# Performance work log

Measured on AMD Instinct MI355X. Metric: run time of the kernel, lower is better.

## Reference

```python
import jax, jax.numpy as jnp
import numpy as np
from math import factorial

DEGREES = 6
REP = 10
PROJ = 64
R = 0.8
B = DEGREES + 1          # bandwidth; spherical signal grid is (2B, 2B)
M = (DEGREES + 1) ** 2   # 49 spherical-harmonic coefficients

# ---------- Wigner small-d coefficient tables (numpy, per degree) ----------

def _wigner_terms(l):
    idx_mp, idx_m, coef, pc, ps = [], [], [], [], []
    for mp in range(-l, l + 1):
        for m in range(-l, l + 1):
            pref = np.sqrt(float(factorial(l + mp) * factorial(l - mp) * factorial(l + m) * factorial(l - m)))
            for k in range(max(0, m - mp), min(l + m, l - mp) + 1):
                c = ((-1.0) ** (mp - m + k)) * pref / (
                    factorial(l + m - k) * factorial(k) * factorial(l - mp - k) * factorial(mp - m + k))
                idx_mp.append(mp + l); idx_m.append(m + l); coef.append(c)
                pc.append(2 * l + m - mp - 2 * k); ps.append(mp - m + 2 * k)
    return (np.asarray(idx_mp), np.asarray(idx_m), np.asarray(coef, np.float32),
            np.asarray(pc, np.float32), np.asarray(ps, np.float32))

_TERMS = [_wigner_terms(l) for l in range(DEGREES + 1)]


def _wigner_d(l, beta):
    """Real Wigner small-d matrix d^l_{m',m}(beta): (n, 2l+1, 2l+1)."""
    imp, im, coef, pc, ps = _TERMS[l]
    c = jnp.cos(beta / 2)[:, None]
    s = jnp.sin(beta / 2)[:, None]
    t = coef[None] * (c ** pc[None]) * (s ** ps[None])   # (n, T)
    d = jnp.zeros((beta.shape[0], 2 * l + 1, 2 * l + 1), beta.dtype)
    return d.at[:, imp, im].add(t)


def rotate_spectrum(angles, spectrum):
    """Block-diagonal complex Wigner-D multiply.
    angles: (n,3) ZYZ Euler; spectrum: (M, rep, 2) -> (Sre, Sim) each (n, M, rep)."""
    alpha, beta, gamma = angles[:, 0], angles[:, 1], angles[:, 2]
    out_re, out_im = [], []
    for l in range(DEGREES + 1):
        d = _wigner_d(l, beta)                                    # (n, 2l+1, 2l+1)
        ms = jnp.arange(-l, l + 1, dtype=angles.dtype)
        ang = ms[None, :, None] * alpha[:, None, None] + ms[None, None, :] * gamma[:, None, None]
        Dre = d * jnp.cos(ang)
        Dim = -d * jnp.sin(ang)                                   # D = e^{-i m' a} d e^{-i m g}
        blk = spectrum[l * l:(l + 1) * (l + 1)]                   # (2l+1, rep, 2)
        Sre, Sim = blk[..., 0], blk[..., 1]
        out_re.append(jnp.einsum('nij,jr->nir', Dre, Sre) - jnp.einsum('nij,jr->nir', Dim, Sim))
        out_im.append(jnp.einsum('nij,jr->nir', Dre, Sim) + jnp.einsum('nij,jr->nir', Dim, Sre))
    return jnp.concatenate(out_re, 1), jnp.concatenate(out_im, 1)


# ---------- Spherical harmonic synthesis table (numpy constant) ----------

def _sph_harm_table():
    J = 2 * B
    betas = np.pi * (2 * np.arange(J) + 1) / (4 * B)
    alphas = 2 * np.pi * np.arange(J) / J
    x, sx = np.cos(betas), np.sin(betas)
    L = DEGREES
    P = np.zeros((L + 1, L + 1, J))   # associated Legendre P[l, m] (Condon-Shortley)
    P[0, 0] = 1.0
    for m in range(1, L + 1):
        P[m, m] = -(2 * m - 1) * sx * P[m - 1, m - 1]
    for m in range(L + 1):
        if m + 1 <= L:
            P[m + 1, m] = (2 * m + 1) * x * P[m, m]
        for l in range(m + 2, L + 1):
            P[l, m] = ((2 * l - 1) * x * P[l - 1, m] - (l + m - 1) * P[l - 2, m]) / (l - m)
    Yre = np.zeros((M, J, J)); Yim = np.zeros((M, J, J))
    for l in range(L + 1):
        for m in range(0, l + 1):
            N = np.sqrt((2 * l + 1) / (4 * np.pi) * factorial(l - m) / factorial(l + m))
            pr = N * P[l, m]
            yre = pr[:, None] * np.cos(m * alphas)[None, :]
            yim = pr[:, None] * np.sin(m * alphas)[None, :]
            Yre[l * l + l + m], Yim[l * l + l + m] = yre, yim
            if m > 0:
                sgn = (-1.0) ** m
                Yre[l * l + l - m], Yim[l * l + l - m] = sgn * yre, -sgn * yim
    return jnp.asarray(Yre, jnp.float32), jnp.asarray(Yim, jnp.float32)

_YRE, _YIM = _sph_harm_table()


def s2_ifft_real(Sre, Sim):
    """f(beta,alpha) = Re[sum_lm c_lm Y_lm]: (n, rep, 2B, 2B)."""
    return jnp.einsum('nmr,mjk->nrjk', Sre, _YRE) - jnp.einsum('nmr,mjk->nrjk', Sim, _YIM)


# ---------- Orthographic sampling grid (numpy constant) ----------

def _ortho_grid(h, w, r):
    ys, xs = np.meshgrid(np.linspace(-r, r, h), np.linspace(-r, r, w), indexing='ij')
    rho = np.sqrt(xs ** 2 + ys ** 2)
    theta = np.arcsin(np.clip(rho, 0.0, 1.0))     # colatitude of front hemisphere
    phi = np.arctan2(ys, xs)                      # longitude in [-pi, pi)
    gx = phi / np.pi                              # alpha axis  -> grid x
    gy = 2 * theta / np.pi - 1                    # beta axis   -> grid y
    return jnp.asarray(np.stack([gx, gy], -1), jnp.float32)

_GRID = _ortho_grid(PROJ, PROJ, R)


def grid_sample_bilinear(img, grid):
    """F.grid_sample(mode=bilinear, padding=zeros, align_corners=False).
    img: (n,C,H,W); grid: (Ho,Wo,2) shared across batch."""
    n, C, H, W = img.shape
    gx = (grid[..., 0] + 1) * W / 2 - 0.5
    gy = (grid[..., 1] + 1) * H / 2 - 0.5
    x0 = jnp.floor(gx); y0 = jnp.floor(gy)
    wx1 = gx - x0; wx0 = 1 - wx1
    wy1 = gy - y0; wy0 = 1 - wy1

    def gather(xi, yi, w):
        valid = (xi >= 0) & (xi < W) & (yi >= 0) & (yi < H)
        xc = jnp.clip(xi, 0, W - 1).astype(jnp.int32)
        yc = jnp.clip(yi, 0, H - 1).astype(jnp.int32)
        vals = img[:, :, yc, xc]                 # (n, C, Ho, Wo)
        return vals * (w * valid)[None, None]
    return (gather(x0, y0, wx0 * wy0) + gather(x0 + 1, y0, wx1 * wy0)
            + gather(x0, y0 + 1, wx0 * wy1) + gather(x0 + 1, y0 + 1, wx1 * wy1))


def deconv_apply(x, wt, bt):
    """ConvTranspose2d(REP,1,kernel=4,stride=2,padding=1); wt torch layout (Cin,Cout,4,4)."""
    k = jnp.transpose(wt[:, :, ::-1, ::-1], (1, 0, 2, 3))   # (Cout,Cin,kh,kw), flipped
    y = jax.lax.conv_general_dilated(x, k, window_strides=(1, 1),
                                     padding=((2, 2), (2, 2)), lhs_dilation=(2, 2),
                                     dimension_numbers=('NCHW', 'OIHW', 'NCHW'))
    return y + bt[None, :, None, None]


def setup_inputs() -> dict:
    key = jax.random.key(0)
    k1, k2, k3 = jax.random.split(key, 3)
    return {
        'angles': jax.random.uniform(k1, (2048, 3), dtype=jnp.float32),
        'spectrum': jax.random.normal(k2, (M, REP, 2), dtype=jnp.float32),
        'wt': jax.random.normal(k3, (REP, 1, 4, 4), dtype=jnp.float32) * 0.1,
        'bt': jnp.zeros((1,), jnp.float32),
    }


def reference(angles, spectrum, wt, bt):
    Sre, Sim = rotate_spectrum(angles, spectrum)        # (n, M, rep) complex parts
    signal = s2_ifft_real(Sre, Sim)                     # (n, rep, 14, 14)
    projection = grid_sample_bilinear(signal, _GRID)    # (n, rep, 64, 64)
    return deconv_apply(projection, wt, bt)             # (n, 1, 128, 128)
```

## Files before the change

kernel.cpp:

```cpp
#include <hip/hip_runtime.h>
#include <math.h>

#define DEG   6
#define MM    49
#define REPC  10
#define JD    14
#define JROWS 8
#define PROJD 64

#define PI_F 3.14159265358979323846f
#define PI_D 3.14159265358979323846

#define WS_GW    0
#define WS_GIDX  17424
#define WS_PT    21780
#define WS_CS    22172
#define WS_FLAG  22368
#define INIT_MAGIC 0x5F3A9C71u

__device__ __constant__ int DOFF[8] = {0,1,10,35,84,165,286,455};
__device__ __constant__ float FACTF[13] = {
    1.f,1.f,2.f,6.f,24.f,120.f,720.f,5040.f,40320.f,362880.f,
    3628800.f,39916800.f,479001600.f};
__device__ __constant__ double FACTD[13] = {
    1.,1.,2.,6.,24.,120.,720.,5040.,40320.,362880.,3628800.,39916800.,479001600.};

__device__ inline float ipowf(float b, int e) {
    float r = 1.f, p = b;
    while (e) { if (e & 1) r *= p; p *= p; e >>= 1; }
    return r;
}

__global__ void init_tables(float* __restrict__ ws) {
    if (*(const volatile unsigned int*)(ws + WS_FLAG) == INIT_MAGIC) return;
    const int tid = blockIdx.x * 256 + threadIdx.x;

    if (tid < 4356) {
        const int ty = tid / 66, tx = tid - ty * 66;
        const int iy = ty - 1, ix = tx - 1;
        float4 wv = make_float4(0.f, 0.f, 0.f, 0.f);
        unsigned int bidx = 0u;
        if ((unsigned)iy < 64u && (unsigned)ix < 64u) {
            float ys = -0.8f + 1.6f * (float)iy / 63.f;
            float xs = -0.8f + 1.6f * (float)ix / 63.f;
            float rho = sqrtf(xs * xs + ys * ys);
            float theta = asinf(fminf(rho, 1.0f));
            float phi = atan2f(ys, xs);
            float gxp = (phi / PI_F + 1.f) * 7.f - 0.5f;
            float gyp = (2.f * theta / PI_F) * 7.f - 0.5f;
            float x0f = floorf(gxp), y0f = floorf(gyp);
            int x0 = (int)x0f, y0 = (int)y0f;
            float fx = gxp - x0f, fy = gyp - y0f;
            float wx0 = 1.f - fx, wx1 = fx, wy0 = 1.f - fy, wy1 = fy;
            int xb = x0, yb = y0;
            if (x0 < 0)            { xb = 0; wx0 = wx1; wx1 = 0.f; }
            else if (x0 >= JD - 1) { wx1 = 0.f; }
            if (y0 < 0)            { yb = 0; wy0 = wy1; wy1 = 0.f; }
            wv = make_float4(wy0*wx0, wy0*wx1, wy1*wx0, wy1*wx1);
            bidx = (unsigned int)((yb * 15 + xb) * 17);
        }
        ((float4*)(ws + WS_GW))[tid] = wv;
        ((unsigned int*)(ws + WS_GIDX))[tid] = bidx;
    }

    const int t2 = tid - 4356;
    if (t2 >= 0 && t2 < JROWS) {
        const int j = t2;
        double bj = PI_D * (2.0 * j + 1.0) / 28.0;
        double x = cos(bj), sx = sin(bj);
        double P[7][7];
        P[0][0] = 1.0;
        for (int m = 1; m <= 6; ++m) P[m][m] = -(2.0*m - 1.0) * sx * P[m-1][m-1];
        for (int m = 0; m <= 6; ++m) {
            if (m + 1 <= 6) P[m+1][m] = (2.0*m + 1.0) * x * P[m][m];
            for (int l = m + 2; l <= 6; ++l)
                P[l][m] = ((2.0*l - 1.0)*x*P[l-1][m] - (double)(l+m-1)*P[l-2][m])
                          / (double)(l - m);
        }
        for (int l = 0; l <= 6; ++l)
            for (int m = 0; m <= 6; ++m) {
                float v = 0.f;
                if (m <= l) {
                    double N = sqrt((2.0*l + 1.0)/(4.0*PI_D) * FACTD[l-m]/FACTD[l+m]);
                    v = (float)(N * P[l][m]);
                }
                ws[WS_PT + j*49 + l*7 + m] = v;
            }
    } else if (t2 >= JROWS && t2 < JROWS + JD) {
        const int k = t2 - JROWS;
        for (int mu = 0; mu <= 6; ++mu) {
            double ang = 2.0 * PI_D * (double)k * (double)mu / 14.0;
            ws[WS_CS + (k*7 + mu)*2 + 0] = (float)cos(ang);
            ws[WS_CS + (k*7 + mu)*2 + 1] = (float)sin(ang);
        }
    }
}

__global__ __launch_bounds__(256, 8) void fused_decode(
    const float* __restrict__ angles,
    const float* __restrict__ spectrum,
    const float* __restrict__ wt,
    const float* __restrict__ bt,
    float* __restrict__ out,
    const float* __restrict__ ws) {
    const int n = blockIdx.x;
    const int tid = threadIdx.x;

    __shared__ float2 Ss[490];
    __shared__ float  T16p[2040];
    __shared__ float  wLc[160];
    __shared__ float  bufU[1772];

    float*  sigL  = bufU;
    float*  dmatL = bufU + 1120;
    float2* CsL   = (float2*)(bufU + 1576);
    float*  specL = T16p;
    float2* ABL   = (float2*)T16p;

    const float alpha = angles[n*3 + 0];
    const float beta  = angles[n*3 + 1];
    const float gamma = angles[n*3 + 2];

    if (tid < 245) ((float4*)specL)[tid] = ((const float4*)spectrum)[tid];
    if (tid < 40)  ((float4*)wLc)[tid]   = ((const float4*)wt)[tid];
    if (tid < 49)  ((float4*)CsL)[tid]   = ((const float4*)(ws + WS_CS))[tid];

    {
        float cb = cosf(beta * 0.5f), sb = sinf(beta * 0.5f);
        float ratio = (sb * sb) / (cb * cb);
        for (int idx = tid; idx < 455; idx += 256) {
            int l = 0;
            while (idx >= DOFF[l+1]) ++l;
            int tl = 2*l + 1;
            int loc = idx - DOFF[l];
            int mp = loc / tl - l;
            int m  = loc % tl - l;
            float pref = sqrtf(FACTF[l+mp]*FACTF[l-mp]*FACTF[l+m]*FACTF[l-m]);
            int k0 = max(0, m - mp), k1 = min(l + m, l - mp);
            float p = ipowf(cb, 2*l + m - mp - 2*k0) * ipowf(sb, mp - m + 2*k0);
            float dsum = 0.f;
            for (int k = k0; k <= k1; ++k) {
                float c = pref / (FACTF[l+m-k]*FACTF[k]*FACTF[l-mp-k]*FACTF[mp-m+k]);
                if ((mp - m + k) & 1) c = -c;
                dsum += c * p;
                p *= ratio;
            }
            dmatL[idx] = dsum;
        }
    }
    __syncthreads();

    {
        float cg, sg; sincosf(gamma, &sg, &cg);
        for (int idx = tid; idx < 490; idx += 256) {
            int lm = idx / 10, r = idx - lm*10;
            int l = 0; { while ((l+1)*(l+1) <= lm) ++l; }
            int mp = lm - l*l - l;
            int tl = 2*l + 1;
            const float* drow = dmatL + DOFF[l] + (mp + l)*tl;
            float ca, sa; sincosf((float)mp*alpha - (float)l*gamma, &sa, &ca);
            float sre = 0.f, sim = 0.f;
            const float* sp = specL + (l*l)*20 + r*2;
            for (int mi = 0; mi < tl; ++mi) {
                float d = drow[mi];
                float Dre = d * ca, Dim = -d * sa;
                float vr = sp[mi*20], vi = sp[mi*20 + 1];
                sre += Dre*vr - Dim*vi;
                sim += Dre*vi + Dim*vr;
                float ca2 = ca*cg - sa*sg;
                float sa2 = sa*cg + ca*sg;
                ca = ca2; sa = sa2;
            }
            Ss[lm*10 + r] = make_float2(sre, sim);
        }
    }
    __syncthreads();

    for (int idx = tid; idx < 560; idx += 256) {
        int r = idx % 10;
        int jm = idx / 10;
        int j = jm / 7, mu = jm - j*7;
        float sgn = (mu & 1) ? -1.f : 1.f;
        const float* pt = ws + WS_PT + j*49 + mu;
        float A = 0.f, B = 0.f;
        #pragma unroll
        for (int l = 0; l <= 6; ++l) {
            float P = pt[l*7];
            int base = l*l + l;
            int im = base - mu; im = im < 0 ? 0 : im;
            float2 spv = Ss[(base + mu)*10 + r];
            float2 snv = Ss[im*10 + r];
            A += P * (spv.x + sgn*snv.x);
            B += P * (sgn*snv.y - spv.y);
        }
        float sc = (mu == 0) ? 0.5f : 1.f;
        ABL[idx] = make_float2(A*sc, B*sc);
    }
    __syncthreads();

    for (int idx = tid; idx < 1120; idx += 256) {
        int k = idx % 14;
        int t = idx / 14;
        int j = t & 7, r = t >> 3;
        const float2* ab = ABL + j*70 + r;
        const float2* cs = CsL + k*7;
        float acc = 0.f;
        #pragma unroll
        for (int mu = 0; mu <= 6; ++mu) {
            float2 a = ab[mu*10];
            float2 c = cs[mu];
            acc += a.x*c.x + a.y*c.y;
        }
        sigL[idx] = acc;
    }
    __syncthreads();

    for (int idx = tid; idx < 1920; idx += 256) {
        int c = idx & 15, p = idx >> 4;
        int j = p / 15, k = p - j*15;
        float acc = 0.f;
        if (k < 14) {
            const float* sl = sigL + j*14 + k;
            const float* wc = wLc + c;
            #pragma unroll
            for (int r = 0; r < REPC; ++r)
                acc += wc[r*16] * sl[r*112];
        }
        T16p[p*17 + c] = acc;
    }
    __syncthreads();

    const float btv = bt[0];
    const int qx  = tid & 127;
    const int qy0 = tid >> 7;
    const int ixh = (qx + 1) >> 1, kxh = (qx + 1) & 1;
    const int kyh = (qy0 + 1) & 1;
    const int iyh0 = (qy0 + 1) >> 1;
    const int cN0 = kyh*4 + kxh, cN1 = cN0 + 2;
    const int cO0 = cN0 + 8,     cO1 = cN0 + 10;
    const int col0 = ixh + 1, col1 = ixh;

    const unsigned int* gI = (const unsigned int*)(ws + WS_GIDX);
    const float4* gWt = (const float4*)(ws + WS_GW);

    int rowO = iyh0 * 66;
    unsigned int bO0 = gI[rowO + col0], bO1 = gI[rowO + col1];
    float4 wO0 = gWt[rowO + col0],  wO1 = gWt[rowO + col1];
    int rowN = rowO + 66;
    unsigned int bN0 = gI[rowN + col0], bN1 = gI[rowN + col1];
    float4 wN0 = gWt[rowN + col0],  wN1 = gWt[rowN + col1];

    float* op = out + (size_t)n * 16384 + qy0 * 128 + qx;

    for (int t = 0; t < 64; ++t) {
        float pN0 = fmaf(wN0.x, T16p[bN0 + cN0],
                    fmaf(wN0.y, T16p[bN0 + 17 + cN0],
                    fmaf(wN0.z, T16p[bN0 + 255 + cN0],
                         wN0.w * T16p[bN0 + 272 + cN0])));
        float pN1 = fmaf(wN1.x, T16p[bN1 + cN1],
                    fmaf(wN1.y, T16p[bN1 + 17 + cN1],
                    fmaf(wN1.z, T16p[bN1 + 255 + cN1],
                         wN1.w * T16p[bN1 + 272 + cN1])));
        float pO0 = fmaf(wO0.x, T16p[bO0 + cO0],
                    fmaf(wO0.y, T16p[bO0 + 17 + cO0],
                    fmaf(wO0.z, T16p[bO0 + 255 + cO0],
                         wO0.w * T16p[bO0 + 272 + cO0])));
        float pO1 = fmaf(wO1.x, T16p[bO1 + cO1],
                    fmaf(wO1.y, T16p[bO1 + 17 + cO1],
                    fmaf(wO1.z, T16p[bO1 + 255 + cO1],
                         wO1.w * T16p[bO1 + 272 + cO1])));
        op[0] = btv + pN0 + pN1 + pO0 + pO1;
        op += 256;

        bO0 = bN0; bO1 = bN1; wO0 = wN0; wO1 = wN1;
        if (t < 63) {
            rowN += 66;
            bN0 = gI[rowN + col0]; bN1 = gI[rowN + col1];
            wN0 = gWt[rowN + col0]; wN1 = gWt[rowN + col1];
        }
    }

    if (n == 0 && tid == 0)
        *((volatile unsigned int*)(ws + WS_FLAG)) = INIT_MAGIC;
}

extern "C" void kernel_launch(void* const* d_in, const int* in_sizes, int n_in,
                              void* d_out, int out_size, void* d_ws, size_t ws_size,
                              hipStream_t stream) {
    const float* angles   = nullptr;
    const float* spectrum = nullptr;
    const float* wt       = nullptr;
    const float* bt       = nullptr;
    int n = 2048;
    for (int i = 0; i < n_in; ++i) {
        int sz = in_sizes[i];
        if (sz == 980)      spectrum = (const float*)d_in[i];
        else if (sz == 160) wt = (const float*)d_in[i];
        else if (sz == 1)   bt = (const float*)d_in[i];
        else { angles = (const float*)d_in[i]; n = sz / 3; }
    }
    float* out = (float*)d_out;
    float* ws  = (float*)d_ws;
    (void)ws_size;

    init_tables<<<18, 256, 0, stream>>>(ws);
    fused_decode<<<n, 256, 0, stream>>>(angles, spectrum, wt, bt, out, ws);
}
```

Baseline: 207.2 us.

## Transpose tap table layout, triple-buffer gather weights, use nontemporal output stores

Changes the T16p shared layout from row-major (j,k) to (k,j) and updates the precomputed gather indices to match. The output loop becomes a 3-way rotating register buffer that prefetches one row ahead, and the init table is enlarged by one row so the extra prefetch stays in bounds. Output writes use nontemporal stores to avoid cache pollution from the 128 MB output stream, and the wt staging moves into the dead Ss buffer to cut LDS usage. The goals are fewer LDS bank conflicts, better load latency hiding and less write-path cache traffic, at the cost of more live registers.

```diff
diff --git a/kernel.cpp b/kernel.cpp
--- a/kernel.cpp
+++ b/kernel.cpp
@@ -12,11 +12,11 @@
 #define PI_D 3.14159265358979323846
 
 #define WS_GW    0
-#define WS_GIDX  17424
-#define WS_PT    21780
-#define WS_CS    22172
-#define WS_FLAG  22368
-#define INIT_MAGIC 0x5F3A9C71u
+#define WS_GIDX  17688
+#define WS_PT    22112
+#define WS_CS    22504
+#define WS_FLAG  22700
+#define INIT_MAGIC 0x5F3A9C72u
 
 __device__ __constant__ int DOFF[8] = {0,1,10,35,84,165,286,455};
 __device__ __constant__ float FACTF[13] = {
@@ -35,7 +35,7 @@
     if (*(const volatile unsigned int*)(ws + WS_FLAG) == INIT_MAGIC) return;
     const int tid = blockIdx.x * 256 + threadIdx.x;
 
-    if (tid < 4356) {
+    if (tid < 4422) {
         const int ty = tid / 66, tx = tid - ty * 66;
         const int iy = ty - 1, ix = tx - 1;
         float4 wv = make_float4(0.f, 0.f, 0.f, 0.f);
@@ -57,13 +57,13 @@
             else if (x0 >= JD - 1) { wx1 = 0.f; }
             if (y0 < 0)            { yb = 0; wy0 = wy1; wy1 = 0.f; }
             wv = make_float4(wy0*wx0, wy0*wx1, wy1*wx0, wy1*wx1);
-            bidx = (unsigned int)((yb * 15 + xb) * 17);
+            bidx = (unsigned int)((xb * 8 + yb) * 17);
         }
         ((float4*)(ws + WS_GW))[tid] = wv;
         ((unsigned int*)(ws + WS_GIDX))[tid] = bidx;
     }
 
-    const int t2 = tid - 4356;
+    const int t2 = tid - 4422;
     if (t2 >= 0 && t2 < JROWS) {
         const int j = t2;
         double bj = PI_D * (2.0 * j + 1.0) / 28.0;
@@ -96,6 +96,15 @@
     }
 }
 
+__device__ __forceinline__ float tap4(const float* __restrict__ T, int b, int c,
+                                      float4 w) {
+    int a = b + c;
+    return fmaf(w.x, T[a],
+           fmaf(w.y, T[a + 136],
+           fmaf(w.z, T[a + 17],
+                w.w * T[a + 153])));
+}
+
 __global__ __launch_bounds__(256, 8) void fused_decode(
     const float* __restrict__ angles,
     const float* __restrict__ spectrum,
@@ -106,23 +115,22 @@
     const int n = blockIdx.x;
     const int tid = threadIdx.x;
 
-    __shared__ float2 Ss[490];
-    __shared__ float  T16p[2040];
-    __shared__ float  wLc[160];
-    __shared__ float  bufU[1772];
+    __shared__ __align__(16) float2 Ss[490];
+    __shared__ __align__(16) float  T16p[2040];
+    __shared__ __align__(16) float  bufU[1772];
 
     float*  sigL  = bufU;
     float*  dmatL = bufU + 1120;
     float2* CsL   = (float2*)(bufU + 1576);
     float*  specL = T16p;
     float2* ABL   = (float2*)T16p;
+    float*  wLcS  = (float*)Ss;
 
     const float alpha = angles[n*3 + 0];
     const float beta  = angles[n*3 + 1];
     const float gamma = angles[n*3 + 2];
 
     if (tid < 245) ((float4*)specL)[tid] = ((const float4*)spectrum)[tid];
-    if (tid < 40)  ((float4*)wLc)[tid]   = ((const float4*)wt)[tid];
     if (tid < 49)  ((float4*)CsL)[tid]   = ((const float4*)(ws + WS_CS))[tid];
 
     {
@@ -198,6 +206,7 @@
     }
     __syncthreads();
 
+    if (tid < 40) ((float4*)wLcS)[tid] = ((const float4*)wt)[tid];
     for (int idx = tid; idx < 1120; idx += 256) {
         int k = idx % 14;
         int t = idx / 14;
@@ -221,12 +230,12 @@
         float acc = 0.f;
         if (k < 14) {
             const float* sl = sigL + j*14 + k;
-            const float* wc = wLc + c;
+            const float* wc = wLcS + c;
             #pragma unroll
             for (int r = 0; r < REPC; ++r)
                 acc += wc[r*16] * sl[r*112];
         }
-        T16p[p*17 + c] = acc;
+        T16p[(k*8 + j)*17 + c] = acc;
     }
     __syncthreads();
 
@@ -238,46 +247,49 @@
     const int iyh0 = (qy0 + 1) >> 1;
     const int cN0 = kyh*4 + kxh, cN1 = cN0 + 2;
     const int cO0 = cN0 + 8,     cO1 = cN0 + 10;
-    const int col0 = ixh + 1, col1 = ixh;
 
     const unsigned int* gI = (const unsigned int*)(ws + WS_GIDX);
     const float4* gWt = (const float4*)(ws + WS_GW);
 
-    int rowO = iyh0 * 66;
-    unsigned int bO0 = gI[rowO + col0], bO1 = gI[rowO + col1];
-    float4 wO0 = gWt[rowO + col0],  wO1 = gWt[rowO + col1];
-    int rowN = rowO + 66;
-    unsigned int bN0 = gI[rowN + col0], bN1 = gI[rowN + col1];
-    float4 wN0 = gWt[rowN + col0],  wN1 = gWt[rowN + col1];
+    int ridx = iyh0 * 66 + (ixh + 1);
+    float4 wA0 = gWt[ridx];   unsigned int bA0 = gI[ridx];
+    float4 wB0 = gWt[ridx-1]; unsigned int bB0 = gI[ridx-1];
+    ridx += 66;
+    float4 wA1 = gWt[ridx];   unsigned int bA1 = gI[ridx];
+    float4 wB1 = gWt[ridx-1]; unsigned int bB1 = gI[ridx-1];
+    ridx += 66;
+    float4 wA2 = gWt[ridx];   unsigned int bA2 = gI[ridx];
+    float4 wB2 = gWt[ridx-1]; unsigned int bB2 = gI[ridx-1];
 
     float* op = out + (size_t)n * 16384 + qy0 * 128 + qx;
 
-    for (int t = 0; t < 64; ++t) {
-        float pN0 = fmaf(wN0.x, T16p[bN0 + cN0],
-                    fmaf(wN0.y, T16p[bN0 + 17 + cN0],
-                    fmaf(wN0.z, T16p[bN0 + 255 + cN0],
-                         wN0.w * T16p[bN0 + 272 + cN0])));
-        float pN1 = fmaf(wN1.x, T16p[bN1 + cN1],
-                    fmaf(wN1.y, T16p[bN1 + 17 + cN1],
-                    fmaf(wN1.z, T16p[bN1 + 255 + cN1],
-                         wN1.w * T16p[bN1 + 272 + cN1])));
-        float pO0 = fmaf(wO0.x, T16p[bO0 + cO0],
-                    fmaf(wO0.y, T16p[bO0 + 17 + cO0],
-                    fmaf(wO0.z, T16p[bO0 + 255 + cO0],
-                         wO0.w * T16p[bO0 + 272 + cO0])));
-        float pO1 = fmaf(wO1.x, T16p[bO1 + cO1],
-                    fmaf(wO1.y, T16p[bO1 + 17 + cO1],
-                    fmaf(wO1.z, T16p[bO1 + 255 + cO1],
-                         wO1.w * T16p[bO1 + 272 + cO1])));
-        op[0] = btv + pN0 + pN1 + pO0 + pO1;
-        op += 256;
-
-        bO0 = bN0; bO1 = bN1; wO0 = wN0; wO1 = wN1;
-        if (t < 63) {
-            rowN += 66;
-            bN0 = gI[rowN + col0]; bN1 = gI[rowN + col1];
-            wN0 = gWt[rowN + col0]; wN1 = gWt[rowN + col1];
-        }
+    for (int t = 0; t < 63; t += 3) {
+        {
+            float o = btv + tap4(T16p, bA1, cN0, wA1) + tap4(T16p, bB1, cN1, wB1)
+                          + tap4(T16p, bA0, cO0, wA0) + tap4(T16p, bB0, cO1, wB0);
+            __builtin_nontemporal_store(o, op); op += 256;
+            ridx += 66;
+            wA0 = gWt[ridx]; bA0 = gI[ridx]; wB0 = gWt[ridx-1]; bB0 = gI[ridx-1];
+        }
+        {
+            float o = btv + tap4(T16p, bA2, cN0, wA2) + tap4(T16p, bB2, cN1, wB2)
+                          + tap4(T16p, bA1, cO0, wA1) + tap4(T16p, bB1, cO1, wB1);
+            __builtin_nontemporal_store(o, op); op += 256;
+            ridx += 66;
+            wA1 = gWt[ridx]; bA1 = gI[ridx]; wB1 = gWt[ridx-1]; bB1 = gI[ridx-1];
+        }
+        {
+            float o = btv + tap4(T16p, bA0, cN0, wA0) + tap4(T16p, bB0, cN1, wB0)
+                          + tap4(T16p, bA2, cO0, wA2) + tap4(T16p, bB2, cO1, wB2);
+            __builtin_nontemporal_store(o, op); op += 256;
+            ridx += 66;
+            wA2 = gWt[ridx]; bA2 = gI[ridx]; wB2 = gWt[ridx-1]; bB2 = gI[ridx-1];
+        }
+    }
+    {
+        float o = btv + tap4(T16p, bA1, cN0, wA1) + tap4(T16p, bB1, cN1, wB1)
+                      + tap4(T16p, bA0, cO0, wA0) + tap4(T16p, bB0, cO1, wB0);
+        __builtin_nontemporal_store(o, op);
     }
 
     if (n == 0 && tid == 0)
```

Result: faster. 199.6 us (-3.7%).
